# Kernel optimization log

Hardware: AMD Instinct MI355X
Metric: run time of the kernel (lower is better)

Reference implementation:

```python
import jax, jax.numpy as jnp
import numpy as np

B, S, T = 16, 256, 2048
V, D, H, L, FF, NM = 3000, 512, 8, 6, 2048, 80
DH = D // H


def _make_pe(max_len=5000, d=D):
    pos = np.arange(max_len, dtype=np.float32)[:, None]
    div = np.exp(np.arange(0, d, 2, dtype=np.float32) * (-np.log(10000.0) / d))
    pe = np.zeros((max_len, d), dtype=np.float32)
    pe[:, 0::2] = np.sin(pos * div)
    pe[:, 1::2] = np.cos(pos * div)
    return jnp.asarray(pe[None])  # [1, max_len, D]


def setup_inputs() -> dict:
    key = jax.random.key(0)
    ks = jax.random.split(key, 24)
    f = jnp.float32
    n = lambda k, sh, s=0.02: jax.random.normal(k, sh, f) * s
    return {
        'text_ids': jax.random.randint(ks[0], (B, S), 0, V),
        'text_lengths': jax.random.randint(ks[1], (B,), S // 2, S + 1),
        'mel_targets': jax.random.normal(ks[2], (B, NM, T), f),
        'emb': n(ks[3], (V, D), 0.05),
        'pe': _make_pe(),
        'Wqkv': n(ks[4], (L, D, 3 * D)), 'bqkv': jnp.zeros((L, 3 * D), f),
        'Wo': n(ks[5], (L, D, D)), 'bo': jnp.zeros((L, D), f),
        'ln1_s': jnp.ones((L, D), f), 'ln1_b': jnp.zeros((L, D), f),
        'ln2_s': jnp.ones((L, D), f), 'ln2_b': jnp.zeros((L, D), f),
        'W1': n(ks[6], (L, D, FF)), 'b1': jnp.zeros((L, FF), f),
        'W2': n(ks[7], (L, FF, D)), 'b2': jnp.zeros((L, D), f),
        'mel_W1': n(ks[8], (D, FF)), 'mel_b1': jnp.zeros((FF,), f),
        'mel_W2': n(ks[9], (FF, NM)), 'mel_b2': jnp.zeros((NM,), f),
        'dur_W1': n(ks[10], (D, 256)), 'dur_b1': jnp.zeros((256,), f),
        'dur_W2': n(ks[11], (256, 1)), 'dur_b2': jnp.zeros((1,), f),
    }


def _layer_norm(x, s, b, eps=1e-5):
    m = jnp.mean(x, -1, keepdims=True)
    v = jnp.mean(jnp.square(x - m), -1, keepdims=True)
    return (x - m) * jax.lax.rsqrt(v + eps) * s + b


def _length_regulate(enc, durations, target_len):
    # enc [B,S,D], durations [B,S] -> [B,target_len,D]
    dur = jnp.maximum(jnp.round(durations).astype(jnp.int32), 1)
    cum = jnp.cumsum(dur, axis=1)                              # [B,S] inclusive
    pos = jnp.arange(target_len)                               # [T]
    idx = jnp.sum(pos[None, None, :] >= cum[:, :, None], axis=1)  # [B,T]
    idx = jnp.minimum(idx, enc.shape[1] - 1)
    valid = pos[None, :] < cum[:, -1:]                         # [B,T]
    out = jnp.take_along_axis(enc, idx[..., None], axis=1)
    return out * valid[..., None].astype(enc.dtype)


def reference(text_ids, text_lengths, mel_targets, emb, pe, Wqkv, bqkv, Wo, bo,
              ln1_s, ln1_b, ln2_s, ln2_b, W1, b1, W2, b2,
              mel_W1, mel_b1, mel_W2, mel_b2, dur_W1, dur_b1, dur_W2, dur_b2):
    x = emb[text_ids] + pe[:, :S]                              # [B,S,D]
    pad = jnp.arange(S)[None, :] >= text_lengths[:, None]      # True = padded key
    bias = jnp.where(pad, -1e9, 0.0)[:, None, None, :]         # [B,1,1,S]
    scale = 1.0 / jnp.sqrt(jnp.float32(DH))
    for l in range(L):
        qkv = x @ Wqkv[l] + bqkv[l]
        q, k, v = jnp.split(qkv, 3, axis=-1)
        q = q.reshape(B, S, H, DH).transpose(0, 2, 1, 3)
        k = k.reshape(B, S, H, DH).transpose(0, 2, 1, 3)
        v = v.reshape(B, S, H, DH).transpose(0, 2, 1, 3)
        scores = jnp.einsum('bhqd,bhkd->bhqk', q, k) * scale + bias
        attn = jax.nn.softmax(scores, axis=-1)
        o = jnp.einsum('bhqk,bhkd->bhqd', attn, v)
        o = o.transpose(0, 2, 1, 3).reshape(B, S, D) @ Wo[l] + bo[l]
        x = _layer_norm(x + o, ln1_s[l], ln1_b[l])              # post-LN (torch default)
        ff = jax.nn.relu(x @ W1[l] + b1[l]) @ W2[l] + b2[l]
        x = _layer_norm(x + ff, ln2_s[l], ln2_b[l])
    enc = x
    dur_h = jax.nn.relu(enc @ dur_W1 + dur_b1)
    durations = jax.nn.softplus((dur_h @ dur_W2 + dur_b2).squeeze(-1))  # [B,S]
    target_len = mel_targets.shape[2]
    expanded = _length_regulate(enc, durations, target_len)    # [B,T,D]
    mel = jax.nn.relu(expanded @ mel_W1 + mel_b1) @ mel_W2 + mel_b2
    mel = mel.transpose(0, 2, 1)                               # [B,NM,T]
    return mel, durations, enc
```

## Files before the change

kernel.cpp:

```cpp
#include <hip/hip_runtime.h>
#include <math.h>

#define B_ 16
#define S_ 256
#define T_ 2048
#define D_ 512
#define H_ 8
#define L_ 6
#define FF_ 2048
#define NM_ 80
#define M_ 4096

typedef float floatx4 __attribute__((ext_vector_type(4)));
typedef __bf16 bf16x8 __attribute__((ext_vector_type(8)));

__device__ __forceinline__ float bf2f(unsigned u) {
    return __uint_as_float((u & 0xffffu) << 16);
}
__device__ __forceinline__ unsigned short f2bf(float f) {
    unsigned u = __float_as_uint(f);
    unsigned r = u + 0x7fffu + ((u >> 16) & 1u);
    return (unsigned short)(r >> 16);
}
__device__ __forceinline__ void gload_lds16(const void* g, void* l) {
    __builtin_amdgcn_global_load_lds(
        (const __attribute__((address_space(1))) void*)g,
        (__attribute__((address_space(3))) void*)l, 16, 0, 0);
}

__global__ __launch_bounds__(256) void transpose_bf16(
    const float* __restrict__ src, unsigned short* __restrict__ dst,
    int K, int N)
{
    __shared__ float tile[32][33];
    const int k0 = blockIdx.y * 32, n0 = blockIdx.x * 32;
    src += (size_t)blockIdx.z * K * N;
    dst += (size_t)blockIdx.z * K * N;
    const int tx = threadIdx.x, ty = threadIdx.y;
#pragma unroll
    for (int i = 0; i < 32; i += 8)
        tile[ty + i][tx] = src[(size_t)(k0 + ty + i) * N + n0 + tx];
    __syncthreads();
#pragma unroll
    for (int i = 0; i < 32; i += 8)
        dst[(size_t)(n0 + ty + i) * K + k0 + tx] = f2bf(tile[tx][ty + i]);
}

__global__ __launch_bounds__(256) void transpose_pad_bf16(
    const float* __restrict__ src, unsigned short* __restrict__ dst,
    int K, int Ns)
{
    __shared__ float tile[32][33];
    const int k0 = blockIdx.y * 32, n0 = blockIdx.x * 32;
    const int tx = threadIdx.x, ty = threadIdx.y;
#pragma unroll
    for (int i = 0; i < 32; i += 8) {
        int n = n0 + tx;
        tile[ty + i][tx] = (n < Ns) ? src[(size_t)(k0 + ty + i) * Ns + n] : 0.f;
    }
    __syncthreads();
#pragma unroll
    for (int i = 0; i < 32; i += 8)
        dst[(size_t)(n0 + ty + i) * K + k0 + tx] = f2bf(tile[tx][ty + i]);
}

__global__ __launch_bounds__(128) void embed_bf16(
    const int* __restrict__ ids, const float* __restrict__ emb,
    const float* __restrict__ pe, unsigned short* __restrict__ x)
{
    const int r = blockIdx.x;
    const int c = threadIdx.x * 4;
    const int id = ids[r];
    const int s = r & (S_ - 1);
    float4 e = *(const float4*)(emb + (size_t)id * D_ + c);
    float4 p = *(const float4*)(pe + (size_t)s * D_ + c);
    ushort4 o;
    o.x = f2bf(e.x + p.x); o.y = f2bf(e.y + p.y);
    o.z = f2bf(e.z + p.z); o.w = f2bf(e.w + p.w);
    *(ushort4*)(x + (size_t)r * D_ + c) = o;
}

template<int BN>
__global__ __launch_bounds__(256) void gemm2(
    const unsigned short* __restrict__ A, const unsigned short* __restrict__ Bt,
    const float* __restrict__ bias, unsigned short* __restrict__ Cb,
    float* __restrict__ Cpart, int N, int klen, int act)
{
    constexpr int NSUB_B = BN / 8;
    constexpr int NSUB = 16 + NSUB_B;
    constexpr int NL = NSUB / 4;
    constexpr int BUFSZ = NSUB * 1024;
    constexpr int WN = BN / 32;
    __shared__ __attribute__((aligned(16))) char smem[2 * BUFSZ];

    const int tid = threadIdx.x;
    const int wave = tid >> 6, lane = tid & 63;
    const int lm = lane & 15, quad = lane >> 4;
    const int wm = wave >> 1, wn = wave & 1;
    const int m0 = blockIdx.y * 128;
    const int n0 = blockIdx.x * BN;
    const int Kfull = klen * gridDim.z;
    const int kb = blockIdx.z * klen;

    floatx4 acc[4][WN];
#pragma unroll
    for (int i = 0; i < 4; i++)
#pragma unroll
        for (int j = 0; j < WN; j++) acc[i][j] = (floatx4){0.f, 0.f, 0.f, 0.f};

    const unsigned short* ga[NL];
    int loff[NL];
#pragma unroll
    for (int j = 0; j < NL; j++) {
        int sid = wave * NL + j;
        if (sid < 16) {
            int mi = sid >> 1, ki = sid & 1;
            ga[j] = A + (size_t)(m0 + mi * 16 + lm) * Kfull + kb + ki * 32 + quad * 8;
            loff[j] = sid * 1024;
        } else {
            int t = sid - 16;
            int ni = t >> 1, ki = t & 1;
            ga[j] = Bt + (size_t)(n0 + ni * 16 + lm) * Kfull + kb + ki * 32 + quad * 8;
            loff[j] = 16384 + t * 1024;
        }
    }

#pragma unroll
    for (int j = 0; j < NL; j++) gload_lds16(ga[j], smem + loff[j]);

    for (int kt = 0; kt < klen; kt += 64) {
        char* sc = smem + ((kt >> 6) & 1) * BUFSZ;
        if (kt + 64 < klen) {
            char* sn = smem + (((kt >> 6) + 1) & 1) * BUFSZ;
#pragma unroll
            for (int j = 0; j < NL; j++) gload_lds16(ga[j] + kt + 64, sn + loff[j]);
            __builtin_amdgcn_s_waitcnt(0x0F70 | NL);
        } else {
            __builtin_amdgcn_s_waitcnt(0x0F70);
        }
        asm volatile("" ::: "memory");
        __builtin_amdgcn_s_barrier();
        asm volatile("" ::: "memory");

#pragma unroll
        for (int ki = 0; ki < 2; ki++) {
            bf16x8 af[4], bfr[WN];
#pragma unroll
            for (int i = 0; i < 4; i++)
                af[i] = *(const bf16x8*)(sc + ((((wm * 4 + i) * 2 + ki) << 10) + (lane << 4)));
#pragma unroll
            for (int j = 0; j < WN; j++)
                bfr[j] = *(const bf16x8*)(sc + 16384 + ((((wn * WN + j) * 2 + ki) << 10) + (lane << 4)));
#pragma unroll
            for (int i = 0; i < 4; i++)
#pragma unroll
                for (int j = 0; j < WN; j++)
                    acc[i][j] = __builtin_amdgcn_mfma_f32_16x16x32_bf16(
                        af[i], bfr[j], acc[i][j], 0, 0, 0);
        }
        asm volatile("" ::: "memory");
        __builtin_amdgcn_s_barrier();
        asm volatile("" ::: "memory");
    }

    if (gridDim.z == 1) {
#pragma unroll
        for (int mi = 0; mi < 4; mi++) {
            const int rb = m0 + wm * 64 + mi * 16 + quad * 4;
#pragma unroll
            for (int nj = 0; nj < WN; nj++) {
                const int col = n0 + wn * (WN * 16) + nj * 16 + lm;
                const float bv = bias[col];
#pragma unroll
                for (int r = 0; r < 4; r++) {
                    float o = acc[mi][nj][r] + bv;
                    if (act) o = fmaxf(o, 0.f);
                    Cb[(size_t)(rb + r) * N + col] = f2bf(o);
                }
            }
        }
    } else {
        float* Cp = Cpart + (size_t)blockIdx.z * gridDim.y * 128 * N;
#pragma unroll
        for (int mi = 0; mi < 4; mi++) {
            const int rb = m0 + wm * 64 + mi * 16 + quad * 4;
#pragma unroll
            for (int nj = 0; nj < WN; nj++) {
                const int col = n0 + wn * (WN * 16) + nj * 16 + lm;
#pragma unroll
                for (int r = 0; r < 4; r++)
                    Cp[(size_t)(rb + r) * N + col] = acc[mi][nj][r];
            }
        }
    }
}

__global__ __launch_bounds__(256) void transpose_v(
    const unsigned short* __restrict__ qkv, unsigned short* __restrict__ vt)
{
    __shared__ unsigned short tile[64][74];
    const int tid = threadIdx.x;
    const int bh = blockIdx.y;
    const int b = bh >> 3, h = bh & 7;
    const int s0 = blockIdx.x * 64;
    const int ty = tid >> 3, tx = tid & 7;
#pragma unroll
    for (int i = 0; i < 64; i += 32) {
        uint4 v = *(const uint4*)(qkv + (size_t)(b * 256 + s0 + ty + i) * 1536
                                  + 1024 + h * 64 + tx * 8);
        unsigned short* dstp = &tile[ty + i][tx * 8];
        const unsigned short* sp = (const unsigned short*)&v;
#pragma unroll
        for (int j = 0; j < 8; j++) dstp[j] = sp[j];
    }
    __syncthreads();
#pragma unroll
    for (int i = 0; i < 64; i += 32) {
        int d = ty + i;
        unsigned short tmp[8];
#pragma unroll
        for (int j = 0; j < 8; j++) tmp[j] = tile[tx * 8 + j][d];
        *(uint4*)(vt + (size_t)(bh * 64 + d) * 256 + s0 + tx * 8) = *(uint4*)tmp;
    }
}

__global__ __launch_bounds__(256) void attn_fused(
    const unsigned short* __restrict__ qkv, const unsigned short* __restrict__ vt,
    const int* __restrict__ lens, unsigned short* __restrict__ o)
{
    __shared__ __attribute__((aligned(16))) char smem[34816];
    const int tid = threadIdx.x;
    const int wave = tid >> 6, lane = tid & 63;
    const int lm = lane & 15, quad = lane >> 4;
    const int qt = blockIdx.x;
    const int bh = blockIdx.y;
    const int b = bh >> 3, h = bh & 7;
    const int len = lens[b];
    const unsigned short* Qb = qkv + ((size_t)b * 256 + qt * 128) * 1536 + h * 64;
    const unsigned short* Kb = qkv + (size_t)b * 256 * 1536 + 512 + h * 64;
    const unsigned short* Vt = vt + (size_t)bh * 64 * 256;

#pragma unroll
    for (int j = 0; j < 8; j++) {
        int sid = wave * 8 + j;
        int nf = sid >> 1, kf = sid & 1;
        gload_lds16(Kb + (size_t)(nf * 16 + lm) * 1536 + kf * 32 + quad * 8,
                    smem + sid * 1024);
    }
    bf16x8 aq[2][2];
#pragma unroll
    for (int mi = 0; mi < 2; mi++)
#pragma unroll
        for (int kf = 0; kf < 2; kf++)
            aq[mi][kf] = *(const bf16x8*)(Qb + (size_t)(wave * 32 + mi * 16 + lm) * 1536
                                          + kf * 32 + quad * 8);
    __syncthreads();

    floatx4 accS[2][16];
#pragma unroll
    for (int mi = 0; mi < 2; mi++)
#pragma unroll
        for (int nf = 0; nf < 16; nf++) accS[mi][nf] = (floatx4){0.f, 0.f, 0.f, 0.f};

#pragma unroll
    for (int nf = 0; nf < 16; nf++) {
        bf16x8 bk0 = *(const bf16x8*)(smem + (nf * 2 + 0) * 1024 + lane * 16);
        bf16x8 bk1 = *(const bf16x8*)(smem + (nf * 2 + 1) * 1024 + lane * 16);
        accS[0][nf] = __builtin_amdgcn_mfma_f32_16x16x32_bf16(aq[0][0], bk0, accS[0][nf], 0, 0, 0);
        accS[0][nf] = __builtin_amdgcn_mfma_f32_16x16x32_bf16(aq[0][1], bk1, accS[0][nf], 0, 0, 0);
        accS[1][nf] = __builtin_amdgcn_mfma_f32_16x16x32_bf16(aq[1][0], bk0, accS[1][nf], 0, 0, 0);
        accS[1][nf] = __builtin_amdgcn_mfma_f32_16x16x32_bf16(aq[1][1], bk1, accS[1][nf], 0, 0, 0);
    }

    float lrow[2][4];
    const float scale = 0.125f;
#pragma unroll
    for (int mi = 0; mi < 2; mi++)
#pragma unroll
        for (int r = 0; r < 4; r++) {
            float mx = -1e30f;
#pragma unroll
            for (int nf = 0; nf < 16; nf++) {
                float s = accS[mi][nf][r] * scale + ((nf * 16 + lm >= len) ? -1e9f : 0.f);
                accS[mi][nf][r] = s;
                mx = fmaxf(mx, s);
            }
#pragma unroll
            for (int off = 1; off < 16; off <<= 1) mx = fmaxf(mx, __shfl_xor(mx, off, 64));
            float sum = 0.f;
#pragma unroll
            for (int nf = 0; nf < 16; nf++) {
                float e = __expf(accS[mi][nf][r] - mx);
                accS[mi][nf][r] = e;
                sum += e;
            }
#pragma unroll
            for (int off = 1; off < 16; off <<= 1) sum += __shfl_xor(sum, off, 64);
            lrow[mi][r] = sum;
        }

    floatx4 accO[2][4];
#pragma unroll
    for (int mi = 0; mi < 2; mi++)
#pragma unroll
        for (int nj = 0; nj < 4; nj++) accO[mi][nj] = (floatx4){0.f, 0.f, 0.f, 0.f};

    unsigned short* sP = (unsigned short*)smem;
    const int rbase = wave * 32;
#pragma unroll
    for (int half = 0; half < 2; half++) {
        __syncthreads();
#pragma unroll
        for (int mi = 0; mi < 2; mi++)
#pragma unroll
            for (int nf2 = 0; nf2 < 8; nf2++) {
                int nf = half * 8 + nf2;
                int row = rbase + mi * 16 + quad * 4;
                int col = nf2 * 16 + lm;
#pragma unroll
                for (int r = 0; r < 4; r++)
                    sP[(row + r) * 136 + col] = f2bf(accS[mi][nf][r]);
            }
        __syncthreads();
#pragma unroll
        for (int ks2 = 0; ks2 < 4; ks2++) {
            bf16x8 ap[2];
#pragma unroll
            for (int mi = 0; mi < 2; mi++)
                ap[mi] = *(const bf16x8*)(sP + (rbase + mi * 16 + lm) * 136
                                          + ks2 * 32 + quad * 8);
            int ks = half * 4 + ks2;
#pragma unroll
            for (int nj = 0; nj < 4; nj++) {
                bf16x8 bv = *(const bf16x8*)(Vt + (size_t)(nj * 16 + lm) * 256
                                             + ks * 32 + quad * 8);
                accO[0][nj] = __builtin_amdgcn_mfma_f32_16x16x32_bf16(ap[0], bv, accO[0][nj], 0, 0, 0);
                accO[1][nj] = __builtin_amdgcn_mfma_f32_16x16x32_bf16(ap[1], bv, accO[1][nj], 0, 0, 0);
            }
        }
    }

#pragma unroll
    for (int mi = 0; mi < 2; mi++) {
        float inv[4];
#pragma unroll
        for (int r = 0; r < 4; r++) inv[r] = 1.f / lrow[mi][r];
        const int grow = b * 256 + qt * 128 + rbase + mi * 16 + quad * 4;
#pragma unroll
        for (int nj = 0; nj < 4; nj++) {
            const int gcol = h * 64 + nj * 16 + lm;
#pragma unroll
            for (int r = 0; r < 4; r++)
                o[(size_t)(grow + r) * 512 + gcol] = f2bf(accO[mi][nj][r] * inv[r]);
        }
    }
}

__global__ __launch_bounds__(128) void add_ln_bf16(
    unsigned short* __restrict__ x, const unsigned short* __restrict__ y,
    const float* __restrict__ s, const float* __restrict__ bb)
{
    __shared__ float red[2];
    const int row = blockIdx.x;
    const int tid = threadIdx.x;
    const int c = tid * 4;
    ushort4 xv = *(const ushort4*)(x + (size_t)row * D_ + c);
    ushort4 yv = *(const ushort4*)(y + (size_t)row * D_ + c);
    float h[4];
    h[0] = bf2f(xv.x) + bf2f(yv.x);
    h[1] = bf2f(xv.y) + bf2f(yv.y);
    h[2] = bf2f(xv.z) + bf2f(yv.z);
    h[3] = bf2f(xv.w) + bf2f(yv.w);

    float sum = h[0] + h[1] + h[2] + h[3];
#pragma unroll
    for (int off = 32; off >= 1; off >>= 1) sum += __shfl_xor(sum, off, 64);
    if ((tid & 63) == 0) red[tid >> 6] = sum;
    __syncthreads();
    float mean = (red[0] + red[1]) * (1.f / 512.f);
    __syncthreads();

    float d[4];
    d[0] = h[0] - mean; d[1] = h[1] - mean; d[2] = h[2] - mean; d[3] = h[3] - mean;
    float sq = d[0] * d[0] + d[1] * d[1] + d[2] * d[2] + d[3] * d[3];
#pragma unroll
    for (int off = 32; off >= 1; off >>= 1) sq += __shfl_xor(sq, off, 64);
    if ((tid & 63) == 0) red[tid >> 6] = sq;
    __syncthreads();
    float var = (red[0] + red[1]) * (1.f / 512.f);
    float rs = rsqrtf(var + 1e-5f);

    float4 sv = *(const float4*)(s + c);
    float4 bv = *(const float4*)(bb + c);
    ushort4 ov;
    ov.x = f2bf(d[0] * rs * sv.x + bv.x);
    ov.y = f2bf(d[1] * rs * sv.y + bv.y);
    ov.z = f2bf(d[2] * rs * sv.z + bv.z);
    ov.w = f2bf(d[3] * rs * sv.w + bv.w);
    *(ushort4*)(x + (size_t)row * D_ + c) = ov;
}

__global__ __launch_bounds__(128) void add_ln_part(
    unsigned short* __restrict__ x, const float* __restrict__ p0,
    const float* __restrict__ p1, const float* __restrict__ bias,
    const float* __restrict__ s, const float* __restrict__ bb,
    float* __restrict__ enc_opt)
{
    __shared__ float red[2];
    const int row = blockIdx.x;
    const int tid = threadIdx.x;
    const int c = tid * 4;
    ushort4 xv = *(const ushort4*)(x + (size_t)row * D_ + c);
    float4 a = *(const float4*)(p0 + (size_t)row * D_ + c);
    float4 bq = *(const float4*)(p1 + (size_t)row * D_ + c);
    float4 bi = *(const float4*)(bias + c);
    float h[4];
    h[0] = bf2f(xv.x) + a.x + bq.x + bi.x;
    h[1] = bf2f(xv.y) + a.y + bq.y + bi.y;
    h[2] = bf2f(xv.z) + a.z + bq.z + bi.z;
    h[3] = bf2f(xv.w) + a.w + bq.w + bi.w;

    float sum = h[0] + h[1] + h[2] + h[3];
#pragma unroll
    for (int off = 32; off >= 1; off >>= 1) sum += __shfl_xor(sum, off, 64);
    if ((tid & 63) == 0) red[tid >> 6] = sum;
    __syncthreads();
    float mean = (red[0] + red[1]) * (1.f / 512.f);
    __syncthreads();

    float d[4];
    d[0] = h[0] - mean; d[1] = h[1] - mean; d[2] = h[2] - mean; d[3] = h[3] - mean;
    float sq = d[0] * d[0] + d[1] * d[1] + d[2] * d[2] + d[3] * d[3];
#pragma unroll
    for (int off = 32; off >= 1; off >>= 1) sq += __shfl_xor(sq, off, 64);
    if ((tid & 63) == 0) red[tid >> 6] = sq;
    __syncthreads();
    float var = (red[0] + red[1]) * (1.f / 512.f);
    float rs = rsqrtf(var + 1e-5f);

    float4 sv = *(const float4*)(s + c);
    float4 bv = *(const float4*)(bb + c);
    float o[4];
    o[0] = d[0] * rs * sv.x + bv.x;
    o[1] = d[1] * rs * sv.y + bv.y;
    o[2] = d[2] * rs * sv.z + bv.z;
    o[3] = d[3] * rs * sv.w + bv.w;
    ushort4 ov;
    ov.x = f2bf(o[0]); ov.y = f2bf(o[1]); ov.z = f2bf(o[2]); ov.w = f2bf(o[3]);
    *(ushort4*)(x + (size_t)row * D_ + c) = ov;
    if (enc_opt) {
        float4 e; e.x = o[0]; e.y = o[1]; e.z = o[2]; e.w = o[3];
        *(float4*)(enc_opt + (size_t)row * D_ + c) = e;
    }
}

__global__ __launch_bounds__(256) void dur_head2(
    const float* __restrict__ p0, const float* __restrict__ p1,
    const float* __restrict__ b1, const float* __restrict__ w2,
    const float* __restrict__ b2, float* __restrict__ durout)
{
    const int tid = threadIdx.x;
    const int w = tid >> 6, lane = tid & 63;
    const int r = blockIdx.x * 4 + w;
    float4 a = *(const float4*)(p0 + (size_t)r * 256 + lane * 4);
    float4 bq = *(const float4*)(p1 + (size_t)r * 256 + lane * 4);
    float4 bi = *(const float4*)(b1 + lane * 4);
    float4 wv = *(const float4*)(w2 + lane * 4);
    float h0 = fmaxf(a.x + bq.x + bi.x, 0.f);
    float h1 = fmaxf(a.y + bq.y + bi.y, 0.f);
    float h2 = fmaxf(a.z + bq.z + bi.z, 0.f);
    float h3 = fmaxf(a.w + bq.w + bi.w, 0.f);
    float p = h0 * wv.x + h1 * wv.y + h2 * wv.z + h3 * wv.w;
#pragma unroll
    for (int off = 32; off >= 1; off >>= 1) p += __shfl_xor(p, off, 64);
    if (lane == 0) {
        float v = p + b2[0];
        durout[r] = (v > 20.f) ? v : log1pf(expf(v));
    }
}

__global__ __launch_bounds__(256) void dur_cumsum(
    const float* __restrict__ dur, int* __restrict__ cum)
{
    __shared__ int sc[256];
    const int b = blockIdx.x, s = threadIdx.x;
    int d = (int)rintf(dur[b * 256 + s]);
    if (d < 1) d = 1;
    sc[s] = d;
    __syncthreads();
    for (int off = 1; off < 256; off <<= 1) {
        int v = sc[s];
        int add = (s >= off) ? sc[s - off] : 0;
        __syncthreads();
        sc[s] = v + add;
        __syncthreads();
    }
    cum[b * 256 + s] = sc[s];
}

__global__ __launch_bounds__(256) void mel_c0(
    const float* __restrict__ b1, const float* __restrict__ W2,
    const float* __restrict__ b2, float* __restrict__ c0)
{
    __shared__ float red[4];
    const int c = blockIdx.x;
    const int tid = threadIdx.x;
    float p = 0.f;
    for (int f = tid; f < 2048; f += 256)
        p += fmaxf(b1[f], 0.f) * W2[(size_t)f * 80 + c];
#pragma unroll
    for (int off = 32; off >= 1; off >>= 1) p += __shfl_xor(p, off, 64);
    if ((tid & 63) == 0) red[tid >> 6] = p;
    __syncthreads();
    if (tid == 0) c0[c] = red[0] + red[1] + red[2] + red[3] + b2[c];
}

__global__ __launch_bounds__(256) void mel_gather(
    const float* __restrict__ mp, const float* __restrict__ b2,
    const float* __restrict__ c0, const int* __restrict__ cum,
    float* __restrict__ mel_out)
{
    __shared__ int sc[256];
    __shared__ float s0[80];
    const int b = blockIdx.y;
    const int t = blockIdx.x * 256 + threadIdx.x;
    sc[threadIdx.x] = cum[b * 256 + threadIdx.x];
    if (threadIdx.x < 80) s0[threadIdx.x] = c0[threadIdx.x];
    __syncthreads();
    const int total = sc[255];
    int lo = 0, hi = 256;
    while (lo < hi) {
        int mid = (lo + hi) >> 1;
        if (sc[mid] <= t) lo = mid + 1; else hi = mid;
    }
    int row = lo < 255 ? lo : 255;
    const bool valid = t < total;
    const size_t base = ((size_t)b * 256 + row) * 128;
    const size_t plane = (size_t)M_ * 128;
    for (int cc = 0; cc < 80; cc++) {
        float v;
        if (valid)
            v = mp[base + cc] + mp[plane + base + cc] + mp[2 * plane + base + cc]
              + mp[3 * plane + base + cc] + b2[cc];
        else
            v = s0[cc];
        mel_out[((size_t)b * 80 + cc) * T_ + t] = v;
    }
}

extern "C" void kernel_launch(void* const* d_in, const int* in_sizes, int n_in,
                              void* d_out, int out_size, void* d_ws, size_t ws_size,
                              hipStream_t stream)
{
    const int*   text_ids     = (const int*)d_in[0];
    const int*   text_lengths = (const int*)d_in[1];
    const float* emb   = (const float*)d_in[3];
    const float* pe    = (const float*)d_in[4];
    const float* Wqkv  = (const float*)d_in[5];
    const float* bqkv  = (const float*)d_in[6];
    const float* Wo    = (const float*)d_in[7];
    const float* bo    = (const float*)d_in[8];
    const float* ln1_s = (const float*)d_in[9];
    const float* ln1_b = (const float*)d_in[10];
    const float* ln2_s = (const float*)d_in[11];
    const float* ln2_b = (const float*)d_in[12];
    const float* W1    = (const float*)d_in[13];
    const float* b1    = (const float*)d_in[14];
    const float* W2    = (const float*)d_in[15];
    const float* b2    = (const float*)d_in[16];
    const float* mel_W1 = (const float*)d_in[17];
    const float* mel_b1 = (const float*)d_in[18];
    const float* mel_W2 = (const float*)d_in[19];
    const float* mel_b2 = (const float*)d_in[20];
    const float* dur_W1 = (const float*)d_in[21];
    const float* dur_b1 = (const float*)d_in[22];
    const float* dur_W2 = (const float*)d_in[23];
    const float* dur_b2 = (const float*)d_in[24];

    float* out = (float*)d_out;
    float* mel_out = out;
    float* dur_out = out + (size_t)B_ * NM_ * T_;
    float* enc_out = dur_out + (size_t)B_ * S_;

    typedef unsigned short u16;
    char* w = (char*)d_ws;
    u16* Wqkv_t  = (u16*)w;                   w += (size_t)L_ * 1536 * 512 * 2;
    u16* Wo_t    = (u16*)w;                   w += (size_t)L_ * 512 * 512 * 2;
    u16* W1_t    = (u16*)w;                   w += (size_t)L_ * 2048 * 512 * 2;
    u16* W2_t    = (u16*)w;                   w += (size_t)L_ * 512 * 2048 * 2;
    u16* melW1_t = (u16*)w;                   w += (size_t)2048 * 512 * 2;
    u16* melW2_t = (u16*)w;                   w += (size_t)128 * 2048 * 2;
    u16* durW1_t = (u16*)w;                   w += (size_t)256 * 512 * 2;
    u16* x_bf    = (u16*)w;                   w += (size_t)M_ * 512 * 2;
    u16* qkv_bf  = (u16*)w;                   w += (size_t)M_ * 1536 * 2;
    u16* ao_bf   = (u16*)w;                   w += (size_t)M_ * 512 * 2;
    u16* y_bf    = (u16*)w;                   w += (size_t)M_ * 512 * 2;
    char* big    = w;                         w += (size_t)16777216;
    float* c0    = (float*)w;                 w += 512;
    int*   cum   = (int*)w;                   w += (size_t)M_ * 4;

    u16* ffh     = (u16*)big;
    u16* melh    = (u16*)big;
    u16* vt      = (u16*)(big + 12582912);

    float* part2 = (float*)qkv_bf;
    float* dpart = (float*)qkv_bf;
    float* mpart = (float*)(qkv_bf + (size_t)M_ * 512);

    transpose_bf16<<<dim3(48, 16, 6), dim3(32, 8), 0, stream>>>(Wqkv, Wqkv_t, 512, 1536);
    transpose_bf16<<<dim3(16, 16, 6), dim3(32, 8), 0, stream>>>(Wo, Wo_t, 512, 512);
    transpose_bf16<<<dim3(64, 16, 6), dim3(32, 8), 0, stream>>>(W1, W1_t, 512, 2048);
    transpose_bf16<<<dim3(16, 64, 6), dim3(32, 8), 0, stream>>>(W2, W2_t, 2048, 512);
    transpose_bf16<<<dim3(64, 16, 1), dim3(32, 8), 0, stream>>>(mel_W1, melW1_t, 512, 2048);
    transpose_pad_bf16<<<dim3(4, 64), dim3(32, 8), 0, stream>>>(mel_W2, melW2_t, 2048, 80);
    transpose_bf16<<<dim3(8, 16, 1), dim3(32, 8), 0, stream>>>(dur_W1, durW1_t, 512, 256);

    embed_bf16<<<M_, 128, 0, stream>>>(text_ids, emb, pe, x_bf);

    for (int l = 0; l < L_; l++) {
        gemm2<128><<<dim3(12, 32), 256, 0, stream>>>(
            x_bf, Wqkv_t + (size_t)l * 1536 * 512, bqkv + (size_t)l * 1536,
            qkv_bf, nullptr, 1536, 512, 0);
        transpose_v<<<dim3(4, 128), 256, 0, stream>>>(qkv_bf, vt);
        attn_fused<<<dim3(2, 128), 256, 0, stream>>>(qkv_bf, vt, text_lengths, ao_bf);
        gemm2<64><<<dim3(8, 32), 256, 0, stream>>>(
            ao_bf, Wo_t + (size_t)l * 512 * 512, bo + (size_t)l * 512,
            y_bf, nullptr, 512, 512, 0);
        add_ln_bf16<<<M_, 128, 0, stream>>>(
            x_bf, y_bf, ln1_s + (size_t)l * D_, ln1_b + (size_t)l * D_);
        gemm2<128><<<dim3(16, 32), 256, 0, stream>>>(
            x_bf, W1_t + (size_t)l * 2048 * 512, b1 + (size_t)l * 2048,
            ffh, nullptr, 2048, 512, 1);
        gemm2<64><<<dim3(8, 32, 2), 256, 0, stream>>>(
            ffh, W2_t + (size_t)l * 512 * 2048, nullptr,
            nullptr, part2, 512, 1024, 0);
        add_ln_part<<<M_, 128, 0, stream>>>(
            x_bf, part2, part2 + (size_t)M_ * 512, b2 + (size_t)l * 512,
            ln2_s + (size_t)l * D_, ln2_b + (size_t)l * D_,
            (l == L_ - 1) ? enc_out : nullptr);
    }

    gemm2<64><<<dim3(4, 32, 2), 256, 0, stream>>>(
        x_bf, durW1_t, nullptr, nullptr, dpart, 256, 256, 0);
    dur_head2<<<M_ / 4, 256, 0, stream>>>(
        dpart, dpart + (size_t)M_ * 256, dur_b1, dur_W2, dur_b2, dur_out);
    dur_cumsum<<<B_, 256, 0, stream>>>(dur_out, cum);

    gemm2<128><<<dim3(16, 32), 256, 0, stream>>>(
        x_bf, melW1_t, mel_b1, melh, nullptr, 2048, 512, 1);
    gemm2<64><<<dim3(2, 32, 4), 256, 0, stream>>>(
        melh, melW2_t, nullptr, nullptr, mpart, 128, 512, 0);
    mel_c0<<<NM_, 256, 0, stream>>>(mel_b1, mel_W2, mel_b2, c0);
    mel_gather<<<dim3(T_ / 256, B_), 256, 0, stream>>>(mpart, mel_b2, c0, cum, mel_out);
}
```

Measured before the change: 919.8 us.

## Shrink GEMM and attention row tiles to raise block count; restructure mel gather

Makes the GEMM M-tile a template parameter and halves it from 128 to 64 rows, doubling the grid for every projection GEMM. Attention now processes 64 query rows per block (one 16-row slice per wave) instead of 128, doubling its grid. The mel gather is split across two channel halves and first reduces the four partial planes into shared memory per batch before the scatter. The aim is better occupancy on the many compute units, at the cost of less operand reuse per block and some redundant partial-sum work in the gather.

```diff
diff --git a/kernel.cpp b/kernel.cpp
--- a/kernel.cpp
+++ b/kernel.cpp
@@ -80,31 +80,33 @@
     *(ushort4*)(x + (size_t)r * D_ + c) = o;
 }
 
-template<int BN>
+template<int BM, int BN>
 __global__ __launch_bounds__(256) void gemm2(
     const unsigned short* __restrict__ A, const unsigned short* __restrict__ Bt,
     const float* __restrict__ bias, unsigned short* __restrict__ Cb,
     float* __restrict__ Cpart, int N, int klen, int act)
 {
+    constexpr int NSUB_A = BM / 8;
     constexpr int NSUB_B = BN / 8;
-    constexpr int NSUB = 16 + NSUB_B;
+    constexpr int NSUB = NSUB_A + NSUB_B;
     constexpr int NL = NSUB / 4;
     constexpr int BUFSZ = NSUB * 1024;
-    constexpr int WN = BN / 32;
+    constexpr int AOFF = NSUB_A * 1024;
+    constexpr int WM = BM / 32, WN = BN / 32;
     __shared__ __attribute__((aligned(16))) char smem[2 * BUFSZ];
 
     const int tid = threadIdx.x;
     const int wave = tid >> 6, lane = tid & 63;
     const int lm = lane & 15, quad = lane >> 4;
     const int wm = wave >> 1, wn = wave & 1;
-    const int m0 = blockIdx.y * 128;
+    const int m0 = blockIdx.y * BM;
     const int n0 = blockIdx.x * BN;
     const int Kfull = klen * gridDim.z;
     const int kb = blockIdx.z * klen;
 
-    floatx4 acc[4][WN];
-#pragma unroll
-    for (int i = 0; i < 4; i++)
+    floatx4 acc[WM][WN];
+#pragma unroll
+    for (int i = 0; i < WM; i++)
 #pragma unroll
         for (int j = 0; j < WN; j++) acc[i][j] = (floatx4){0.f, 0.f, 0.f, 0.f};
 
@@ -113,15 +115,15 @@
 #pragma unroll
     for (int j = 0; j < NL; j++) {
         int sid = wave * NL + j;
-        if (sid < 16) {
+        if (sid < NSUB_A) {
             int mi = sid >> 1, ki = sid & 1;
             ga[j] = A + (size_t)(m0 + mi * 16 + lm) * Kfull + kb + ki * 32 + quad * 8;
             loff[j] = sid * 1024;
         } else {
-            int t = sid - 16;
+            int t = sid - NSUB_A;
             int ni = t >> 1, ki = t & 1;
             ga[j] = Bt + (size_t)(n0 + ni * 16 + lm) * Kfull + kb + ki * 32 + quad * 8;
-            loff[j] = 16384 + t * 1024;
+            loff[j] = AOFF + t * 1024;
         }
     }
 
@@ -144,15 +146,15 @@
 
 #pragma unroll
         for (int ki = 0; ki < 2; ki++) {
-            bf16x8 af[4], bfr[WN];
-#pragma unroll
-            for (int i = 0; i < 4; i++)
-                af[i] = *(const bf16x8*)(sc + ((((wm * 4 + i) * 2 + ki) << 10) + (lane << 4)));
+            bf16x8 af[WM], bfr[WN];
+#pragma unroll
+            for (int i = 0; i < WM; i++)
+                af[i] = *(const bf16x8*)(sc + ((((wm * WM + i) * 2 + ki) << 10) + (lane << 4)));
 #pragma unroll
             for (int j = 0; j < WN; j++)
-                bfr[j] = *(const bf16x8*)(sc + 16384 + ((((wn * WN + j) * 2 + ki) << 10) + (lane << 4)));
-#pragma unroll
-            for (int i = 0; i < 4; i++)
+                bfr[j] = *(const bf16x8*)(sc + AOFF + ((((wn * WN + j) * 2 + ki) << 10) + (lane << 4)));
+#pragma unroll
+            for (int i = 0; i < WM; i++)
 #pragma unroll
                 for (int j = 0; j < WN; j++)
                     acc[i][j] = __builtin_amdgcn_mfma_f32_16x16x32_bf16(
@@ -165,8 +167,8 @@
 
     if (gridDim.z == 1) {
 #pragma unroll
-        for (int mi = 0; mi < 4; mi++) {
-            const int rb = m0 + wm * 64 + mi * 16 + quad * 4;
+        for (int mi = 0; mi < WM; mi++) {
+            const int rb = m0 + wm * (WM * 16) + mi * 16 + quad * 4;
 #pragma unroll
             for (int nj = 0; nj < WN; nj++) {
                 const int col = n0 + wn * (WN * 16) + nj * 16 + lm;
@@ -180,10 +182,10 @@
             }
         }
     } else {
-        float* Cp = Cpart + (size_t)blockIdx.z * gridDim.y * 128 * N;
-#pragma unroll
-        for (int mi = 0; mi < 4; mi++) {
-            const int rb = m0 + wm * 64 + mi * 16 + quad * 4;
+        float* Cp = Cpart + (size_t)blockIdx.z * gridDim.y * BM * N;
+#pragma unroll
+        for (int mi = 0; mi < WM; mi++) {
+            const int rb = m0 + wm * (WM * 16) + mi * 16 + quad * 4;
 #pragma unroll
             for (int nj = 0; nj < WN; nj++) {
                 const int col = n0 + wn * (WN * 16) + nj * 16 + lm;
@@ -228,7 +230,7 @@
     const unsigned short* __restrict__ qkv, const unsigned short* __restrict__ vt,
     const int* __restrict__ lens, unsigned short* __restrict__ o)
 {
-    __shared__ __attribute__((aligned(16))) char smem[34816];
+    __shared__ __attribute__((aligned(16))) char smem[32768];
     const int tid = threadIdx.x;
     const int wave = tid >> 6, lane = tid & 63;
     const int lm = lane & 15, quad = lane >> 4;
@@ -236,9 +238,10 @@
     const int bh = blockIdx.y;
     const int b = bh >> 3, h = bh & 7;
     const int len = lens[b];
-    const unsigned short* Qb = qkv + ((size_t)b * 256 + qt * 128) * 1536 + h * 64;
+    const unsigned short* Qb = qkv + ((size_t)b * 256 + qt * 64) * 1536 + h * 64;
     const unsigned short* Kb = qkv + (size_t)b * 256 * 1536 + 512 + h * 64;
     const unsigned short* Vt = vt + (size_t)bh * 64 * 256;
+    const int rbase = wave * 16;
 
 #pragma unroll
     for (int j = 0; j < 8; j++) {
@@ -247,112 +250,90 @@
         gload_lds16(Kb + (size_t)(nf * 16 + lm) * 1536 + kf * 32 + quad * 8,
                     smem + sid * 1024);
     }
-    bf16x8 aq[2][2];
-#pragma unroll
-    for (int mi = 0; mi < 2; mi++)
-#pragma unroll
-        for (int kf = 0; kf < 2; kf++)
-            aq[mi][kf] = *(const bf16x8*)(Qb + (size_t)(wave * 32 + mi * 16 + lm) * 1536
-                                          + kf * 32 + quad * 8);
-    __syncthreads();
-
-    floatx4 accS[2][16];
-#pragma unroll
-    for (int mi = 0; mi < 2; mi++)
-#pragma unroll
-        for (int nf = 0; nf < 16; nf++) accS[mi][nf] = (floatx4){0.f, 0.f, 0.f, 0.f};
+    bf16x8 aq[2];
+#pragma unroll
+    for (int kf = 0; kf < 2; kf++)
+        aq[kf] = *(const bf16x8*)(Qb + (size_t)(rbase + lm) * 1536 + kf * 32 + quad * 8);
+    __syncthreads();
+
+    floatx4 accS[16];
+#pragma unroll
+    for (int nf = 0; nf < 16; nf++) accS[nf] = (floatx4){0.f, 0.f, 0.f, 0.f};
 
 #pragma unroll
     for (int nf = 0; nf < 16; nf++) {
         bf16x8 bk0 = *(const bf16x8*)(smem + (nf * 2 + 0) * 1024 + lane * 16);
         bf16x8 bk1 = *(const bf16x8*)(smem + (nf * 2 + 1) * 1024 + lane * 16);
-        accS[0][nf] = __builtin_amdgcn_mfma_f32_16x16x32_bf16(aq[0][0], bk0, accS[0][nf], 0, 0, 0);
-        accS[0][nf] = __builtin_amdgcn_mfma_f32_16x16x32_bf16(aq[0][1], bk1, accS[0][nf], 0, 0, 0);
-        accS[1][nf] = __builtin_amdgcn_mfma_f32_16x16x32_bf16(aq[1][0], bk0, accS[1][nf], 0, 0, 0);
-        accS[1][nf] = __builtin_amdgcn_mfma_f32_16x16x32_bf16(aq[1][1], bk1, accS[1][nf], 0, 0, 0);
-    }
-
-    float lrow[2][4];
+        accS[nf] = __builtin_amdgcn_mfma_f32_16x16x32_bf16(aq[0], bk0, accS[nf], 0, 0, 0);
+        accS[nf] = __builtin_amdgcn_mfma_f32_16x16x32_bf16(aq[1], bk1, accS[nf], 0, 0, 0);
+    }
+
+    float lrow[4];
     const float scale = 0.125f;
 #pragma unroll
-    for (int mi = 0; mi < 2; mi++)
-#pragma unroll
-        for (int r = 0; r < 4; r++) {
-            float mx = -1e30f;
-#pragma unroll
-            for (int nf = 0; nf < 16; nf++) {
-                float s = accS[mi][nf][r] * scale + ((nf * 16 + lm >= len) ? -1e9f : 0.f);
-                accS[mi][nf][r] = s;
-                mx = fmaxf(mx, s);
-            }
-#pragma unroll
-            for (int off = 1; off < 16; off <<= 1) mx = fmaxf(mx, __shfl_xor(mx, off, 64));
-            float sum = 0.f;
-#pragma unroll
-            for (int nf = 0; nf < 16; nf++) {
-                float e = __expf(accS[mi][nf][r] - mx);
-                accS[mi][nf][r] = e;
-                sum += e;
-            }
-#pragma unroll
-            for (int off = 1; off < 16; off <<= 1) sum += __shfl_xor(sum, off, 64);
-            lrow[mi][r] = sum;
-        }
-
-    floatx4 accO[2][4];
-#pragma unroll
-    for (int mi = 0; mi < 2; mi++)
-#pragma unroll
-        for (int nj = 0; nj < 4; nj++) accO[mi][nj] = (floatx4){0.f, 0.f, 0.f, 0.f};
+    for (int r = 0; r < 4; r++) {
+        float mx = -1e30f;
+#pragma unroll
+        for (int nf = 0; nf < 16; nf++) {
+            float s = accS[nf][r] * scale + ((nf * 16 + lm >= len) ? -1e9f : 0.f);
+            accS[nf][r] = s;
+            mx = fmaxf(mx, s);
+        }
+#pragma unroll
+        for (int off = 1; off < 16; off <<= 1) mx = fmaxf(mx, __shfl_xor(mx, off, 64));
+        float sum = 0.f;
+#pragma unroll
+        for (int nf = 0; nf < 16; nf++) {
+            float e = __expf(accS[nf][r] - mx);
+            accS[nf][r] = e;
+            sum += e;
+        }
+#pragma unroll
+        for (int off = 1; off < 16; off <<= 1) sum += __shfl_xor(sum, off, 64);
+        lrow[r] = sum;
+    }
+
+    floatx4 accO[4];
+#pragma unroll
+    for (int nj = 0; nj < 4; nj++) accO[nj] = (floatx4){0.f, 0.f, 0.f, 0.f};
 
     unsigned short* sP = (unsigned short*)smem;
-    const int rbase = wave * 32;
 #pragma unroll
     for (int half = 0; half < 2; half++) {
         __syncthreads();
 #pragma unroll
-        for (int mi = 0; mi < 2; mi++)
-#pragma unroll
-            for (int nf2 = 0; nf2 < 8; nf2++) {
-                int nf = half * 8 + nf2;
-                int row = rbase + mi * 16 + quad * 4;
-                int col = nf2 * 16 + lm;
-#pragma unroll
-                for (int r = 0; r < 4; r++)
-                    sP[(row + r) * 136 + col] = f2bf(accS[mi][nf][r]);
-            }
+        for (int nf2 = 0; nf2 < 8; nf2++) {
+            int nf = half * 8 + nf2;
+            int row = rbase + quad * 4;
+            int col = nf2 * 16 + lm;
+#pragma unroll
+            for (int r = 0; r < 4; r++)
+                sP[(row + r) * 136 + col] = f2bf(accS[nf][r]);
+        }
         __syncthreads();
 #pragma unroll
         for (int ks2 = 0; ks2 < 4; ks2++) {
-            bf16x8 ap[2];
-#pragma unroll
-            for (int mi = 0; mi < 2; mi++)
-                ap[mi] = *(const bf16x8*)(sP + (rbase + mi * 16 + lm) * 136
-                                          + ks2 * 32 + quad * 8);
+            bf16x8 ap = *(const bf16x8*)(sP + (rbase + lm) * 136 + ks2 * 32 + quad * 8);
             int ks = half * 4 + ks2;
 #pragma unroll
             for (int nj = 0; nj < 4; nj++) {
                 bf16x8 bv = *(const bf16x8*)(Vt + (size_t)(nj * 16 + lm) * 256
                                              + ks * 32 + quad * 8);
-                accO[0][nj] = __builtin_amdgcn_mfma_f32_16x16x32_bf16(ap[0], bv, accO[0][nj], 0, 0, 0);
-                accO[1][nj] = __builtin_amdgcn_mfma_f32_16x16x32_bf16(ap[1], bv, accO[1][nj], 0, 0, 0);
+                accO[nj] = __builtin_amdgcn_mfma_f32_16x16x32_bf16(ap, bv, accO[nj], 0, 0, 0);
             }
         }
     }
 
-#pragma unroll
-    for (int mi = 0; mi < 2; mi++) {
-        float inv[4];
-#pragma unroll
-        for (int r = 0; r < 4; r++) inv[r] = 1.f / lrow[mi][r];
-        const int grow = b * 256 + qt * 128 + rbase + mi * 16 + quad * 4;
-#pragma unroll
-        for (int nj = 0; nj < 4; nj++) {
-            const int gcol = h * 64 + nj * 16 + lm;
-#pragma unroll
-            for (int r = 0; r < 4; r++)
-                o[(size_t)(grow + r) * 512 + gcol] = f2bf(accO[mi][nj][r] * inv[r]);
-        }
+    float inv[4];
+#pragma unroll
+    for (int r = 0; r < 4; r++) inv[r] = 1.f / lrow[r];
+    const int grow = b * 256 + qt * 64 + rbase + quad * 4;
+#pragma unroll
+    for (int nj = 0; nj < 4; nj++) {
+        const int gcol = h * 64 + nj * 16 + lm;
+#pragma unroll
+        for (int r = 0; r < 4; r++)
+            o[(size_t)(grow + r) * 512 + gcol] = f2bf(accO[nj][r] * inv[r]);
     }
 }
 
@@ -515,19 +496,29 @@
     if (tid == 0) c0[c] = red[0] + red[1] + red[2] + red[3] + b2[c];
 }
 
-__global__ __launch_bounds__(256) void mel_gather(
+__global__ __launch_bounds__(256) void mel_gather2(
     const float* __restrict__ mp, const float* __restrict__ b2,
     const float* __restrict__ c0, const int* __restrict__ cum,
     float* __restrict__ mel_out)
 {
+    __shared__ float rows[256 * 40];
     __shared__ int sc[256];
-    __shared__ float s0[80];
-    const int b = blockIdx.y;
-    const int t = blockIdx.x * 256 + threadIdx.x;
-    sc[threadIdx.x] = cum[b * 256 + threadIdx.x];
-    if (threadIdx.x < 80) s0[threadIdx.x] = c0[threadIdx.x];
+    __shared__ float s0[40];
+    const int tid = threadIdx.x;
+    const int b = blockIdx.z;
+    const int cc0 = blockIdx.y * 40;
+    sc[tid] = cum[b * 256 + tid];
+    if (tid < 40) s0[tid] = c0[cc0 + tid];
+    const size_t plane = (size_t)M_ * 128;
+    for (int idx = tid; idx < 256 * 40; idx += 256) {
+        int r = idx / 40, c = idx - r * 40;
+        size_t base = ((size_t)b * 256 + r) * 128 + cc0 + c;
+        rows[idx] = mp[base] + mp[plane + base] + mp[2 * plane + base]
+                  + mp[3 * plane + base] + b2[cc0 + c];
+    }
     __syncthreads();
     const int total = sc[255];
+    const int t = blockIdx.x * 256 + tid;
     int lo = 0, hi = 256;
     while (lo < hi) {
         int mid = (lo + hi) >> 1;
@@ -535,17 +526,9 @@
     }
     int row = lo < 255 ? lo : 255;
     const bool valid = t < total;
-    const size_t base = ((size_t)b * 256 + row) * 128;
-    const size_t plane = (size_t)M_ * 128;
-    for (int cc = 0; cc < 80; cc++) {
-        float v;
-        if (valid)
-            v = mp[base + cc] + mp[plane + base + cc] + mp[2 * plane + base + cc]
-              + mp[3 * plane + base + cc] + b2[cc];
-        else
-            v = s0[cc];
-        mel_out[((size_t)b * 80 + cc) * T_ + t] = v;
-    }
+    const float* src = valid ? &rows[row * 40] : s0;
+    for (int cc = 0; cc < 40; cc++)
+        mel_out[((size_t)b * 80 + cc0 + cc) * T_ + t] = src[cc];
 }
 
 extern "C" void kernel_launch(void* const* d_in, const int* in_sizes, int n_in,
@@ -618,20 +601,20 @@
     embed_bf16<<<M_, 128, 0, stream>>>(text_ids, emb, pe, x_bf);
 
     for (int l = 0; l < L_; l++) {
-        gemm2<128><<<dim3(12, 32), 256, 0, stream>>>(
+        gemm2<64, 128><<<dim3(12, 64), 256, 0, stream>>>(
             x_bf, Wqkv_t + (size_t)l * 1536 * 512, bqkv + (size_t)l * 1536,
             qkv_bf, nullptr, 1536, 512, 0);
         transpose_v<<<dim3(4, 128), 256, 0, stream>>>(qkv_bf, vt);
-        attn_fused<<<dim3(2, 128), 256, 0, stream>>>(qkv_bf, vt, text_lengths, ao_bf);
-        gemm2<64><<<dim3(8, 32), 256, 0, stream>>>(
+        attn_fused<<<dim3(4, 128), 256, 0, stream>>>(qkv_bf, vt, text_lengths, ao_bf);
+        gemm2<64, 64><<<dim3(8, 64), 256, 0, stream>>>(
             ao_bf, Wo_t + (size_t)l * 512 * 512, bo + (size_t)l * 512,
             y_bf, nullptr, 512, 512, 0);
         add_ln_bf16<<<M_, 128, 0, stream>>>(
             x_bf, y_bf, ln1_s + (size_t)l * D_, ln1_b + (size_t)l * D_);
-        gemm2<128><<<dim3(16, 32), 256, 0, stream>>>(
+        gemm2<64, 128><<<dim3(16, 64), 256, 0, stream>>>(
             x_bf, W1_t + (size_t)l * 2048 * 512, b1 + (size_t)l * 2048,
             ffh, nullptr, 2048, 512, 1);
-        gemm2<64><<<dim3(8, 32, 2), 256, 0, stream>>>(
+        gemm2<64, 64><<<dim3(8, 64, 2), 256, 0, stream>>>(
             ffh, W2_t + (size_t)l * 512 * 2048, nullptr,
             nullptr, part2, 512, 1024, 0);
         add_ln_part<<<M_, 128, 0, stream>>>(
@@ -640,16 +623,16 @@
             (l == L_ - 1) ? enc_out : nullptr);
     }
 
-    gemm2<64><<<dim3(4, 32, 2), 256, 0, stream>>>(
+    gemm2<64, 64><<<dim3(4, 64, 2), 256, 0, stream>>>(
         x_bf, durW1_t, nullptr, nullptr, dpart, 256, 256, 0);
     dur_head2<<<M_ / 4, 256, 0, stream>>>(
         dpart, dpart + (size_t)M_ * 256, dur_b1, dur_W2, dur_b2, dur_out);
     dur_cumsum<<<B_, 256, 0, stream>>>(dur_out, cum);
 
-    gemm2<128><<<dim3(16, 32), 256, 0, stream>>>(
+    gemm2<64, 128><<<dim3(16, 64), 256, 0, stream>>>(
         x_bf, melW1_t, mel_b1, melh, nullptr, 2048, 512, 1);
-    gemm2<64><<<dim3(2, 32, 4), 256, 0, stream>>>(
+    gemm2<64, 128><<<dim3(1, 64, 4), 256, 0, stream>>>(
         melh, melW2_t, nullptr, nullptr, mpart, 128, 512, 0);
     mel_c0<<<NM_, 256, 0, stream>>>(mel_b1, mel_W2, mel_b2, c0);
-    mel_gather<<<dim3(T_ / 256, B_), 256, 0, stream>>>(mpart, mel_b2, c0, cum, mel_out);
-}
+    mel_gather2<<<dim3(T_ / 256, 2, B_), 256, 0, stream>>>(mpart, mel_b2, c0, cum, mel_out);
+}
```

Result: slower. 993.8 us (+8.0%).
